# Optimization experiments

Hardware: AMD Instinct MI355X
Metric: run time of the kernel (lower is better)

The kernel has to match this reference:

```python
import jax, jax.numpy as jnp
import numpy as np

H = 512          # hidden_size
HALF = 256       # hidden_size // 2 (RGCN feature dim)
NHEAD = 8
NLAYER = 12
NBLOCK = 2
NENT = 50000
NREL = 12
NBASES = 8
NEDGE = 500000
TXTD = 768       # raw text/image feature dim
BATCH, ELEN, SLEN = 32, 50, 128


def setup_inputs() -> dict:
    key = jax.random.key(0)
    ks = jax.random.split(key, 40)
    def p(i, shape, scale=0.02):
        return jax.random.normal(ks[i], shape, jnp.float32) * scale
    inp = {
        'entity_ids': jax.random.randint(ks[0], (BATCH, ELEN), 0, NENT),
        'token_embeds': jax.random.normal(ks[1], (BATCH, SLEN, H), jnp.float32),
        'edge_index': jax.random.randint(ks[2], (2, NEDGE), 0, NENT),
        'edge_type': jax.random.randint(ks[3], (NEDGE,), 0, NREL),
        'node_embeds': p(4, (NENT, HALF)),
        'rgcn_basis': p(5, (NBASES, HALF, HALF)),
        'rgcn_comp': p(6, (NREL, NBASES), 0.3),
        'rgcn_root': p(7, (HALF, HALF)),
        'rgcn_bias': p(8, (HALF,)),
        'kg_proj_w': p(9, (HALF, H)), 'kg_proj_b': p(10, (H,)),
        'text_proj_w': p(11, (TXTD, H)), 'text_proj_b': p(12, (H,)),
        'image_proj_w': p(13, (TXTD, H)), 'image_proj_b': p(14, (H,)),
        'cq_w': p(15, (H, H)), 'cq_b': p(16, (H,)),
        'kgk_w': p(17, (H, H)), 'kgk_b': p(18, (H,)),
        'imk_w': p(19, (H, H)), 'imk_b': p(20, (H,)),
        'txk_w': p(21, (H, H)), 'txk_b': p(22, (H,)),
        'pp1_w1': p(23, (H, HALF)), 'pp1_b1': p(24, (HALF,)),
        'pp1_w2': p(25, (HALF, H)), 'pp1_b2': p(26, (H,)),
        'pp2_w': p(27, (H, NLAYER * NBLOCK * H)), 'pp2_b': p(28, (NLAYER * NBLOCK * H,)),
        'text_embeds_init': p(29, (NENT, TXTD), 1.0),
        'image_embeds_init': p(30, (NENT, TXTD), 1.0),
    }
    return inp


def _rgcn(x, edge_index, edge_type, basis, comp, root, bias):
    # PyG RGCNConv with basis decomposition, aggr='mean', root weight + bias.
    # mean_{e: rel=r, dst=i}(x[src_e] @ W_r) == (mean_{e}(x[src_e])) @ W_r, so we
    # aggregate raw features per (dst, relation) segment then apply W_r once per node.
    N = x.shape[0]
    src, dst = edge_index[0], edge_index[1]
    seg = dst * NREL + edge_type                      # combined (node, relation) key
    msgs = x[src]                                     # [E, HALF] gather
    agg = jax.ops.segment_sum(msgs, seg, num_segments=N * NREL)
    cnt = jax.ops.segment_sum(jnp.ones((src.shape[0],), x.dtype), seg, num_segments=N * NREL)
    mean = (agg / jnp.maximum(cnt, 1.0)[:, None]).reshape(N, NREL, HALF)
    w_rel = jnp.einsum('rb,bio->rio', comp, basis)    # [R, HALF, HALF]
    out = jnp.einsum('nri,rio->no', mean, w_rel) + x @ root + bias
    return out


def reference(entity_ids, token_embeds, edge_index, edge_type, node_embeds,
              rgcn_basis, rgcn_comp, rgcn_root, rgcn_bias,
              kg_proj_w, kg_proj_b, text_proj_w, text_proj_b,
              image_proj_w, image_proj_b, cq_w, cq_b,
              kgk_w, kgk_b, imk_w, imk_b, txk_w, txk_b,
              pp1_w1, pp1_b1, pp1_w2, pp1_b2, pp2_w, pp2_b,
              text_embeds_init, image_embeds_init):
    kg_all = _rgcn(node_embeds, edge_index, edge_type, rgcn_basis, rgcn_comp, rgcn_root, rgcn_bias)
    kg_all = kg_all @ kg_proj_w + kg_proj_b           # [N, H]
    kg_feat = kg_all[entity_ids]                      # [B, L, H]
    text_feat = text_embeds_init[entity_ids] @ text_proj_w + text_proj_b
    image_feat = image_embeds_init[entity_ids] @ image_proj_w + image_proj_b
    # context-guided fusion
    q = (jnp.mean(token_embeds, axis=1) @ cq_w + cq_b)[:, None, :]   # [B, 1, H]
    kg_s = jnp.sum(q * (kg_feat @ kgk_w + kgk_b), -1, keepdims=True)
    img_s = jnp.sum(q * (image_feat @ imk_w + imk_b), -1, keepdims=True)
    txt_s = jnp.sum(q * (text_feat @ txk_w + txk_b), -1, keepdims=True)
    w = jax.nn.softmax(jnp.concatenate([kg_s, img_s, txt_s], axis=-1), axis=-1)
    fused = w[..., 0:1] * kg_feat + w[..., 1:2] * image_feat + w[..., 2:3] * text_feat
    # prompt expansion
    h = jax.nn.relu(fused @ pp1_w1 + pp1_b1) @ pp1_w2 + pp1_b2 + fused
    p = h @ pp2_w + pp2_b                             # [B, L, NLAYER*NBLOCK*H]
    B, L = entity_ids.shape
    p = p.reshape(B, L, NLAYER, NBLOCK, NHEAD, H // NHEAD)
    p = jnp.transpose(p, (2, 3, 0, 4, 1, 5))          # [layer, block, B, head, L, head_dim]
    loss_cl = jnp.float32(0.0)                        # output_entity=False path
    return p, loss_cl
```

## Files before the change

kernel.cpp:

```cpp
#include <hip/hip_runtime.h>

#define HDIM 512
#define HALF 256
#define NRELS 12
#define NBASES 8
#define NLAYERS 12
#define NBLOCKS 2
#define NHEADS 8
#define NENTS 50000
#define TXTD 768
#define BATCH 32
#define ELEN 50
#define SLEN 128
#define NPOS (BATCH * ELEN)
#define NSEG (NPOS * NRELS)
#define BCAP 64

typedef unsigned short u16;
typedef __attribute__((ext_vector_type(8))) __bf16 bf16x8;
typedef __attribute__((ext_vector_type(4))) float f32x4;

__device__ __forceinline__ u16 f2bf(float f) {
    unsigned int u = __float_as_uint(f);
    unsigned int r = (u + 0x7FFFu + ((u >> 16) & 1u)) >> 16;
    return (u16)r;
}
__device__ __forceinline__ float bf2f(u16 v) {
    return __uint_as_float(((unsigned int)v) << 16);
}

#define ASYNC_COPY16(g, l)                                                              \
    __builtin_amdgcn_global_load_lds((const __attribute__((address_space(1))) void*)(g), \
                                     (__attribute__((address_space(3))) unsigned int*)(l), 16, 0, 0)

__global__ void init_kernel(int* __restrict__ map, int* __restrict__ segcnt,
                            int* __restrict__ nuniq, float* __restrict__ zb,
                            const float* __restrict__ kgb, const float* __restrict__ imb,
                            const float* __restrict__ txb, u16* __restrict__ SW,
                            const float* __restrict__ rgcn_bias,
                            const float* __restrict__ kg_proj_w,
                            const float* __restrict__ kg_proj_b,
                            float* __restrict__ biasC, float* __restrict__ out_last) {
    int blk = blockIdx.x;
    int t = threadIdx.x;
    if (blk >= 128) {
        int n = (blk - 128) * 256 + t;
        float acc = kg_proj_b[n];
        for (int c = 0; c < HALF; ++c) acc += rgcn_bias[c] * kg_proj_w[(size_t)c * HDIM + n];
        biasC[n] = acc;
        return;
    }
    int tid = blk * 256 + t;
    const int nt = 128 * 256;
    int4 m4 = {-1, -1, -1, -1};
    for (int i = tid; i < NENTS / 4; i += nt) ((int4*)map)[i] = m4;
    int4 z4 = {0, 0, 0, 0};
    for (int i = tid; i < NSEG / 4; i += nt) ((int4*)segcnt)[i] = z4;
    for (int i = tid; i < 2304; i += nt) zb[i] = 0.f;
    if (tid < HDIM) {
        SW[(size_t)1536 * HDIM + tid] = f2bf(kgb[tid]);
        SW[(size_t)1537 * HDIM + tid] = f2bf(imb[tid]);
        SW[(size_t)1538 * HDIM + tid] = f2bf(txb[tid]);
    }
    if (tid == 0) { *nuniq = 0; *out_last = 0.f; }
}

__global__ void dedup_kernel(const int* __restrict__ eid, int* __restrict__ map,
                             int* __restrict__ uniq, int* __restrict__ nuniq) {
    int i = blockIdx.x * blockDim.x + threadIdx.x;
    if (i >= NPOS) return;
    int n = eid[i];
    int old = atomicCAS(&map[n], -1, -2);
    if (old == -1) {
        int idx = atomicAdd(nuniq, 1);
        uniq[idx] = n;
        __threadfence();
        map[n] = idx;
    }
}

struct PrepArgs {
    const float* src[12];
    u16* dst[12];
};

__global__ __launch_bounds__(256) void midprep_kernel(
    const float* __restrict__ tok, u16* __restrict__ TMEAN,
    const int* __restrict__ uniq, const int* __restrict__ nuniq,
    const float* __restrict__ txi, const float* __restrict__ imi,
    u16* __restrict__ TXIN, u16* __restrict__ IMIN,
    const int* __restrict__ ei, const int* __restrict__ et, const int* __restrict__ map,
    int* __restrict__ segcnt, int* __restrict__ bucket, int E, PrepArgs a) {
    int blk = blockIdx.x;
    int t = threadIdx.x;
    if (blk < 64) {
        int b = blk >> 1;
        int col = (blk & 1) * 256 + t;
        float s = 0.f;
        for (int si = 0; si < SLEN; ++si) s += tok[((size_t)b * SLEN + si) * HDIM + col];
        TMEAN[(size_t)b * HDIM + col] = f2bf(s * (1.0f / SLEN));
    } else if (blk < 352) {
        if (t >= TXTD / 4) return;
        int nu = *nuniq;
        for (int u = blk - 64; u < NPOS; u += 288) {
            if (u >= nu) {
                ushort4 z = {0, 0, 0, 0};
                ((ushort4*)(TXIN + (size_t)u * TXTD))[t] = z;
                ((ushort4*)(IMIN + (size_t)u * TXTD))[t] = z;
                continue;
            }
            int n = uniq[u];
            float4 v = ((const float4*)(txi + (size_t)n * TXTD))[t];
            ushort4 o;
            o.x = f2bf(v.x); o.y = f2bf(v.y); o.z = f2bf(v.z); o.w = f2bf(v.w);
            ((ushort4*)(TXIN + (size_t)u * TXTD))[t] = o;
            v = ((const float4*)(imi + (size_t)n * TXTD))[t];
            o.x = f2bf(v.x); o.y = f2bf(v.y); o.z = f2bf(v.z); o.w = f2bf(v.w);
            ((ushort4*)(IMIN + (size_t)u * TXTD))[t] = o;
        }
    } else if (blk < 1024) {
        const int* __restrict__ dstA = ei + E;
        int tid0 = (blk - 352) * 256 + t;
        const int stride = 672 * 256;
        for (int e = tid0; e < E; e += stride) {
            int c = map[dstA[e]];
            if (c >= 0) {
                int seg = c * NRELS + et[e];
                int p = atomicAdd(&segcnt[seg], 1);
                if (p < BCAP) bucket[seg * BCAP + p] = ei[e];
            }
        }
    } else {
        constexpr int NN[7]  = {512, 512, 512, 256, 512, 12288, 512};
        constexpr int LDT[7] = {256, 768, 768, 512, 256, 512, 512};
        constexpr int BASE[13] = {0, 128, 512, 896, 1024, 1152, 7296,
                                  7552, 8064, 8128, 8384, 8640, 8896};
        __shared__ u16 tb[32][33];
        int bid = blk - 1024;
        int op = 0;
        #pragma unroll
        for (int i = 1; i < 12; ++i)
            if (bid >= BASE[i]) op = i;
        int idx = bid - BASE[op];
        if (op < 7) {
            int Nv = 0, ldt = 0;
            #pragma unroll
            for (int i = 0; i < 7; ++i)
                if (op == i) { Nv = NN[i]; ldt = LDT[i]; }
            int ncols = Nv / 32;
            int n0 = (idx % ncols) * 32, k0 = (idx / ncols) * 32;
            const float* W = a.src[op];
            u16* WT = a.dst[op];
            int tx = t & 31, ty = t >> 5;
            #pragma unroll
            for (int i = ty; i < 32; i += 8)
                tb[i][tx] = f2bf(W[(size_t)(k0 + i) * Nv + n0 + tx]);
            __syncthreads();
            #pragma unroll
            for (int i = ty; i < 32; i += 8)
                WT[(size_t)(n0 + i) * ldt + k0 + tx] = tb[tx][i];
        } else {
            int e = idx * 1024 + t * 4;
            float4 v = *(const float4*)(a.src[op] + e);
            ushort4 o;
            o.x = f2bf(v.x); o.y = f2bf(v.y); o.z = f2bf(v.z); o.w = f2bf(v.w);
            *(ushort4*)(a.dst[op] + e) = o;
        }
    }
}

template <int BM, int BN, int WM, int WN, bool SCATTER>
__device__ __forceinline__ void gemm_body(const u16* __restrict__ A, const u16* __restrict__ BT,
                                          const float* __restrict__ bias,
                                          void* __restrict__ Cout, int M, int N, int K,
                                          int bx, int by, bool outbf) {
    constexpr int MF = WM / 16, NF = WN / 16;
    constexpr int NWC = BN / WN;
    __shared__ u16 ldsA[BM][64];
    __shared__ u16 ldsB[BN][64];
    const int tid = threadIdx.x;
    const int lane = tid & 63;
    const int wv = tid >> 6;
    const int m0 = by * BM;
    const int n0 = bx * BN;
    const int wr = wv / NWC, wc = wv % NWC;
    const int srow = lane >> 3;
    const int sslot = lane & 7;

    f32x4 acc[MF][NF];
    #pragma unroll
    for (int i = 0; i < MF; ++i)
        #pragma unroll
        for (int j = 0; j < NF; ++j)
            #pragma unroll
            for (int r = 0; r < 4; ++r) acc[i][j][r] = 0.f;

    for (int k0 = 0; k0 < K; k0 += 64) {
        #pragma unroll
        for (int i = 0; i < BM / 32; ++i) {
            int R = wv * (BM / 4) + i * 8 + srow;
            int gm = m0 + R;
            gm = gm < M ? gm : M - 1;
            int s = sslot ^ (R & 7);
            ASYNC_COPY16(A + (size_t)gm * K + k0 + s * 8, &ldsA[wv * (BM / 4) + i * 8][0]);
        }
        #pragma unroll
        for (int i = 0; i < BN / 32; ++i) {
            int R = wv * (BN / 4) + i * 8 + srow;
            int s = sslot ^ (R & 7);
            ASYNC_COPY16(BT + (size_t)(n0 + R) * K + k0 + s * 8, &ldsB[wv * (BN / 4) + i * 8][0]);
        }
        __syncthreads();
        #pragma unroll
        for (int ks = 0; ks < 2; ++ks) {
            bf16x8 af[MF], bf[NF];
            int kg = ks * 4 + (lane >> 4);
            int rl = lane & 15;
            #pragma unroll
            for (int i = 0; i < MF; ++i) {
                int row = wr * WM + i * 16 + rl;
                af[i] = *(const bf16x8*)&ldsA[row][(kg ^ (row & 7)) * 8];
            }
            #pragma unroll
            for (int j = 0; j < NF; ++j) {
                int row = wc * WN + j * 16 + rl;
                bf[j] = *(const bf16x8*)&ldsB[row][(kg ^ (row & 7)) * 8];
            }
            #pragma unroll
            for (int i = 0; i < MF; ++i)
                #pragma unroll
                for (int j = 0; j < NF; ++j)
                    acc[i][j] = __builtin_amdgcn_mfma_f32_16x16x32_bf16(af[i], bf[j], acc[i][j], 0, 0, 0);
        }
        __syncthreads();
    }

    const int rl = lane & 15, rg = lane >> 4;
    #pragma unroll
    for (int i = 0; i < MF; ++i) {
        #pragma unroll
        for (int j = 0; j < NF; ++j) {
            int col = n0 + wc * WN + j * 16 + rl;
            float bv = bias[col];
            #pragma unroll
            for (int r = 0; r < 4; ++r) {
                int row = m0 + wr * WM + i * 16 + rg * 4 + r;
                if (row >= M) continue;
                float x = acc[i][j][r] + bv;
                if (SCATTER) {
                    int layer = col >> 10, blk = (col >> 9) & 1, head = (col >> 6) & 7, hd = col & 63;
                    int bb = row / ELEN, ll = row - bb * ELEN;
                    size_t oi = (((((size_t)layer * NBLOCKS + blk) * BATCH + bb) * NHEADS + head) * ELEN + ll) * 64 + hd;
                    ((float*)Cout)[oi] = x;
                } else if (outbf) {
                    ((u16*)Cout)[(size_t)row * N + col] = f2bf(x);
                } else {
                    ((float*)Cout)[(size_t)row * N + col] = x;
                }
            }
        }
    }
}

struct BuildArgs {
    const int *segcnt, *bucket, *uniq, *nuniq;
    const float *comp, *x;
    u16* MBX;
    const u16 *TMEAN, *CQT;
    const float* cq_b;
    u16* QB;
    const u16 *KGT, *W1f;
    const float* ZB;
    u16* WC;
    const u16 *TXIN, *TXT, *IMIN, *IMT;
    const float *txb, *imb;
    u16 *TXU, *IMU;
};
__global__ __launch_bounds__(256) void build_kernel(BuildArgs a) {
    int blk = blockIdx.x;
    if (blk >= NPOS) {
        const u16 *A, *BT;
        const float* bias;
        u16* C;
        int M, N, K, bx, by;
        if (blk >= NPOS + 8 + 288 + 200) {
            int i = blk - (NPOS + 8 + 288 + 200);
            A = a.IMIN; BT = a.IMT; bias = a.imb; C = a.IMU;
            M = NPOS; N = HDIM; K = TXTD; bx = i % 8; by = i / 8;
        } else if (blk >= NPOS + 8 + 288) {
            int i = blk - (NPOS + 8 + 288);
            A = a.TXIN; BT = a.TXT; bias = a.txb; C = a.TXU;
            M = NPOS; N = HDIM; K = TXTD; bx = i % 8; by = i / 8;
        } else if (blk >= NPOS + 8) {
            int i = blk - (NPOS + 8);
            A = a.KGT; BT = a.W1f; bias = a.ZB; C = a.WC;
            M = HDIM; N = 2304; K = HALF; bx = i % 36; by = i / 36;
        } else {
            A = a.TMEAN; BT = a.CQT; bias = a.cq_b; C = a.QB;
            M = BATCH; N = HDIM; K = HDIM; bx = blk - NPOS; by = 0;
        }
        gemm_body<64, 64, 32, 32, false>(A, BT, bias, C, M, N, K, bx, by, true);
        return;
    }
    int u = blk;
    int i = threadIdx.x;
    __shared__ float sc[NRELS * NBASES];
    if (i < NRELS * NBASES) sc[i] = a.comp[i];
    __syncthreads();
    u16* row = a.MBX + (size_t)u * 2304;
    int nu = *a.nuniq;
    if (u >= nu) {
        for (int b = 0; b < NBASES + 1; ++b) row[b * HALF + i] = 0;
        return;
    }
    float mr[NRELS];
    #pragma unroll
    for (int r = 0; r < NRELS; ++r) {
        int seg = u * NRELS + r;
        int c = a.segcnt[seg];
        int n = min(c, BCAP);
        float acc = 0.f;
        for (int e = 0; e < n; ++e) {
            int s = a.bucket[seg * BCAP + e];
            acc += a.x[(size_t)s * HALF + i];
        }
        mr[r] = acc * (1.f / fmaxf((float)c, 1.f));
    }
    #pragma unroll
    for (int b = 0; b < NBASES; ++b) {
        float v = 0.f;
        #pragma unroll
        for (int r = 0; r < NRELS; ++r) v += sc[r * NBASES + b] * mr[r];
        row[b * HALF + i] = f2bf(v);
    }
    row[NBASES * HALF + i] = f2bf(a.x[(size_t)a.uniq[u] * HALF + i]);
}

struct ProjArgs {
    const u16 *MBX, *WC, *QB, *SW;
    const float *biasC, *ZB;
    u16* KGU;
    float* QP;
};
__global__ __launch_bounds__(256) void proj_kernel(ProjArgs a) {
    int b = blockIdx.x;
    if (b < 200) {
        gemm_body<64, 64, 32, 32, false>(a.MBX, a.WC, a.biasC, a.KGU,
                                         NPOS, HDIM, 2304, b % 8, b / 8, true);
    } else {
        gemm_body<64, 64, 32, 32, false>(a.QB, a.SW, a.ZB, a.QP,
                                         BATCH, 1600, HDIM, b - 200, 0, false);
    }
}

__global__ __launch_bounds__(256) void tail_kernel(
    const int* __restrict__ eid, const int* __restrict__ map,
    const u16* __restrict__ KGU, const u16* __restrict__ IMU, const u16* __restrict__ TXU,
    const float* __restrict__ qp,
    const u16* __restrict__ W1T, const float* __restrict__ pp1_b1,
    const u16* __restrict__ W2T, const float* __restrict__ pp1_b2,
    u16* __restrict__ Hh) {
    __shared__ u16 FUS[16][520];
    __shared__ u16 P1s[16][264];
    const int bm0 = blockIdx.x * 16;
    const int lane = threadIdx.x & 63;
    const int wv = threadIdx.x >> 6;

    for (int rr = wv; rr < 16; rr += 4) {
        int bl = bm0 + rr;
        int b = bl / ELEN;
        int u = map[eid[bl]];
        const u16* kg = KGU + (size_t)u * HDIM;
        const u16* im = IMU + (size_t)u * HDIM;
        const u16* tx = TXU + (size_t)u * HDIM;
        const float* qrow = qp + (size_t)b * 1600;
        float pkg = 0.f, pim = 0.f, ptx = 0.f;
        for (int e = lane; e < HDIM; e += 64) {
            pkg += bf2f(kg[e]) * qrow[e];
            pim += bf2f(im[e]) * qrow[512 + e];
            ptx += bf2f(tx[e]) * qrow[1024 + e];
        }
        #pragma unroll
        for (int off = 32; off; off >>= 1) {
            pkg += __shfl_down(pkg, off);
            pim += __shfl_down(pim, off);
            ptx += __shfl_down(ptx, off);
        }
        float w0, w1, w2;
        if (lane == 0) {
            float av = pkg + qrow[1536];
            float c1 = pim + qrow[1537];
            float c2 = ptx + qrow[1538];
            float mx = fmaxf(av, fmaxf(c1, c2));
            float ea = __expf(av - mx), eb = __expf(c1 - mx), ec = __expf(c2 - mx);
            float inv = 1.f / (ea + eb + ec);
            w0 = ea * inv; w1 = eb * inv; w2 = ec * inv;
        }
        w0 = __shfl(w0, 0); w1 = __shfl(w1, 0); w2 = __shfl(w2, 0);
        for (int e = lane; e < HDIM; e += 64) {
            float v = w0 * bf2f(kg[e]) + w1 * bf2f(im[e]) + w2 * bf2f(tx[e]);
            FUS[rr][e] = f2bf(v);
        }
    }
    __syncthreads();

    {
        const int rl = lane & 15;
        const int kgrp = lane >> 4;
        f32x4 acc[4];
        #pragma unroll
        for (int j = 0; j < 4; ++j)
            #pragma unroll
            for (int r = 0; r < 4; ++r) acc[j][r] = 0.f;
        for (int kk = 0; kk < 512; kk += 32) {
            int k8 = kk + kgrp * 8;
            bf16x8 af = *(const bf16x8*)&FUS[rl][k8];
            bf16x8 bf[4];
            #pragma unroll
            for (int j = 0; j < 4; ++j) {
                int n = wv * 64 + j * 16 + rl;
                bf[j] = *(const bf16x8*)&W1T[(size_t)n * 512 + k8];
            }
            #pragma unroll
            for (int j = 0; j < 4; ++j)
                acc[j] = __builtin_amdgcn_mfma_f32_16x16x32_bf16(af, bf[j], acc[j], 0, 0, 0);
        }
        const int rg = lane >> 4;
        #pragma unroll
        for (int j = 0; j < 4; ++j) {
            int col = wv * 64 + j * 16 + rl;
            float bv = pp1_b1[col];
            #pragma unroll
            for (int r = 0; r < 4; ++r) {
                int row = rg * 4 + r;
                P1s[row][col] = f2bf(fmaxf(acc[j][r] + bv, 0.f));
            }
        }
    }
    __syncthreads();

    {
        const int rl = lane & 15;
        const int kgrp = lane >> 4;
        f32x4 acc[8];
        #pragma unroll
        for (int j = 0; j < 8; ++j)
            #pragma unroll
            for (int r = 0; r < 4; ++r) acc[j][r] = 0.f;
        for (int kk = 0; kk < 256; kk += 32) {
            int k8 = kk + kgrp * 8;
            bf16x8 af = *(const bf16x8*)&P1s[rl][k8];
            bf16x8 bf[8];
            #pragma unroll
            for (int j = 0; j < 8; ++j) {
                int n = wv * 128 + j * 16 + rl;
                bf[j] = *(const bf16x8*)&W2T[(size_t)n * 256 + k8];
            }
            #pragma unroll
            for (int j = 0; j < 8; ++j)
                acc[j] = __builtin_amdgcn_mfma_f32_16x16x32_bf16(af, bf[j], acc[j], 0, 0, 0);
        }
        const int rg = lane >> 4;
        #pragma unroll
        for (int j = 0; j < 8; ++j) {
            int col = wv * 128 + j * 16 + rl;
            float bv = pp1_b2[col];
            #pragma unroll
            for (int r = 0; r < 4; ++r) {
                int row = rg * 4 + r;
                float v = acc[j][r] + bv + bf2f(FUS[row][col]);
                Hh[(size_t)(bm0 + row) * HDIM + col] = f2bf(v);
            }
        }
    }
}

__global__ __launch_bounds__(256)
void pp2_kernel(const u16* __restrict__ A, const u16* __restrict__ BT,
                const float* __restrict__ bias, void* __restrict__ Cout,
                int M, int N, int K) {
    int id = blockIdx.x;
    int xcd = id & 7;
    int local = id >> 3;
    int bx = xcd * 12 + local % 12;
    int by = local / 12;
    gemm_body<128, 128, 64, 64, true>(A, BT, bias, Cout, M, N, K, bx, by, false);
}

extern "C" void kernel_launch(void* const* d_in, const int* in_sizes, int n_in,
                              void* d_out, int out_size, void* d_ws, size_t ws_size,
                              hipStream_t stream) {
    const int* entity_ids = (const int*)d_in[0];
    const float* token_embeds = (const float*)d_in[1];
    const int* edge_index = (const int*)d_in[2];
    const int* edge_type = (const int*)d_in[3];
    const float* node_embeds = (const float*)d_in[4];
    const float* rgcn_basis = (const float*)d_in[5];
    const float* rgcn_comp = (const float*)d_in[6];
    const float* rgcn_root = (const float*)d_in[7];
    const float* rgcn_bias = (const float*)d_in[8];
    const float* kg_proj_w = (const float*)d_in[9];
    const float* kg_proj_b = (const float*)d_in[10];
    const float* text_proj_w = (const float*)d_in[11];
    const float* text_proj_b = (const float*)d_in[12];
    const float* image_proj_w = (const float*)d_in[13];
    const float* image_proj_b = (const float*)d_in[14];
    const float* cq_w = (const float*)d_in[15];
    const float* cq_b = (const float*)d_in[16];
    const float* kgk_w = (const float*)d_in[17];
    const float* imk_w = (const float*)d_in[19];
    const float* txk_w = (const float*)d_in[21];
    const float* pp1_w1 = (const float*)d_in[23];
    const float* pp1_b1 = (const float*)d_in[24];
    const float* pp1_w2 = (const float*)d_in[25];
    const float* pp1_b2 = (const float*)d_in[26];
    const float* pp2_w = (const float*)d_in[27];
    const float* pp2_b = (const float*)d_in[28];
    const float* text_init = (const float*)d_in[29];
    const float* image_init = (const float*)d_in[30];

    const int E = in_sizes[3];

    size_t off = 0;
    auto alloc = [&](size_t bytes) { size_t o = off; off += (bytes + 255) & ~(size_t)255; return o; };
    char* ws = (char*)d_ws;
    size_t map_o  = alloc((size_t)NENTS * 4);
    size_t nun_o  = alloc(4);
    size_t unq_o  = alloc((size_t)NPOS * 4);
    size_t scnt_o = alloc((size_t)NSEG * 4);
    size_t bkt_o  = alloc((size_t)NSEG * BCAP * 4);
    size_t mbx_o  = alloc((size_t)NPOS * 2304 * 2);
    size_t w1f_o  = alloc((size_t)2304 * HALF * 2);
    size_t wc_o   = alloc((size_t)HDIM * 2304 * 2);
    size_t bc_o   = alloc((size_t)HDIM * 4);
    size_t kgt_o  = alloc((size_t)HDIM * HALF * 2);
    size_t kgu_o  = alloc((size_t)NPOS * HDIM * 2);
    size_t txin_o = alloc((size_t)NPOS * TXTD * 2);
    size_t imin_o = alloc((size_t)NPOS * TXTD * 2);
    size_t txt_o  = alloc((size_t)HDIM * TXTD * 2);
    size_t imt_o  = alloc((size_t)HDIM * TXTD * 2);
    size_t txu_o  = alloc((size_t)NPOS * HDIM * 2);
    size_t imu_o  = alloc((size_t)NPOS * HDIM * 2);
    size_t tm_o   = alloc((size_t)BATCH * HDIM * 2);
    size_t qb_o   = alloc((size_t)BATCH * HDIM * 2);
    size_t cqt_o  = alloc((size_t)HDIM * HDIM * 2);
    size_t sw_o   = alloc((size_t)1600 * HDIM * 2);
    size_t qp_o   = alloc((size_t)BATCH * 1600 * 4);
    size_t zb_o   = alloc((size_t)2304 * 4);
    size_t w1t_o  = alloc((size_t)HALF * HDIM * 2);
    size_t w2t_o  = alloc((size_t)HDIM * HALF * 2);
    size_t h_o    = alloc((size_t)NPOS * HDIM * 2);
    size_t pp2t_o = alloc((size_t)12288 * HDIM * 2);
    if (off > ws_size) return;

    int* map = (int*)(ws + map_o);
    int* nuniq = (int*)(ws + nun_o);
    int* uniq = (int*)(ws + unq_o);
    int* segcnt = (int*)(ws + scnt_o);
    int* bucket = (int*)(ws + bkt_o);
    u16* MBX = (u16*)(ws + mbx_o);
    u16* W1f = (u16*)(ws + w1f_o);
    u16* WC  = (u16*)(ws + wc_o);
    float* biasC = (float*)(ws + bc_o);
    u16* KGT = (u16*)(ws + kgt_o);
    u16* KGU = (u16*)(ws + kgu_o);
    u16* TXIN = (u16*)(ws + txin_o);
    u16* IMIN = (u16*)(ws + imin_o);
    u16* TXT = (u16*)(ws + txt_o);
    u16* IMT = (u16*)(ws + imt_o);
    u16* TXU = (u16*)(ws + txu_o);
    u16* IMU = (u16*)(ws + imu_o);
    u16* TMEAN = (u16*)(ws + tm_o);
    u16* QB  = (u16*)(ws + qb_o);
    u16* CQT = (u16*)(ws + cqt_o);
    u16* SW  = (u16*)(ws + sw_o);
    float* QP  = (float*)(ws + qp_o);
    float* ZB  = (float*)(ws + zb_o);
    u16* W1T = (u16*)(ws + w1t_o);
    u16* W2T = (u16*)(ws + w2t_o);
    u16* Hh  = (u16*)(ws + h_o);
    u16* PP2T = (u16*)(ws + pp2t_o);
    float* OUT = (float*)d_out;

    init_kernel<<<130, 256, 0, stream>>>(map, segcnt, nuniq, ZB,
                                         (const float*)d_in[18], (const float*)d_in[20],
                                         (const float*)d_in[22], SW,
                                         rgcn_bias, kg_proj_w, kg_proj_b, biasC,
                                         OUT + (out_size - 1));
    dedup_kernel<<<(NPOS + 255) / 256, 256, 0, stream>>>(entity_ids, map, uniq, nuniq);
    PrepArgs pa;
    pa.src[0] = kg_proj_w;    pa.dst[0] = KGT;
    pa.src[1] = text_proj_w;  pa.dst[1] = TXT;
    pa.src[2] = image_proj_w; pa.dst[2] = IMT;
    pa.src[3] = pp1_w1;       pa.dst[3] = W1T;
    pa.src[4] = pp1_w2;       pa.dst[4] = W2T;
    pa.src[5] = pp2_w;        pa.dst[5] = PP2T;
    pa.src[6] = cq_w;         pa.dst[6] = CQT;
    pa.src[7] = rgcn_basis;   pa.dst[7] = W1f;
    pa.src[8] = rgcn_root;    pa.dst[8] = W1f + (size_t)2048 * HALF;
    pa.src[9] = kgk_w;        pa.dst[9] = SW;
    pa.src[10] = imk_w;       pa.dst[10] = SW + (size_t)HDIM * HDIM;
    pa.src[11] = txk_w;       pa.dst[11] = SW + (size_t)2 * HDIM * HDIM;
    midprep_kernel<<<9920, 256, 0, stream>>>(token_embeds, TMEAN,
                                             uniq, nuniq, text_init, image_init, TXIN, IMIN,
                                             edge_index, edge_type, map, segcnt, bucket, E, pa);
    BuildArgs ba;
    ba.segcnt = segcnt; ba.bucket = bucket; ba.uniq = uniq; ba.nuniq = nuniq;
    ba.comp = rgcn_comp; ba.x = node_embeds; ba.MBX = MBX;
    ba.TMEAN = TMEAN; ba.CQT = CQT; ba.cq_b = cq_b; ba.QB = QB;
    ba.KGT = KGT; ba.W1f = W1f; ba.ZB = ZB; ba.WC = WC;
    ba.TXIN = TXIN; ba.TXT = TXT; ba.IMIN = IMIN; ba.IMT = IMT;
    ba.txb = text_proj_b; ba.imb = image_proj_b; ba.TXU = TXU; ba.IMU = IMU;
    build_kernel<<<NPOS + 8 + 288 + 400, 256, 0, stream>>>(ba);
    ProjArgs pr;
    pr.MBX = MBX; pr.WC = WC; pr.biasC = biasC; pr.KGU = KGU;
    pr.QB = QB; pr.SW = SW; pr.ZB = ZB; pr.QP = QP;
    proj_kernel<<<225, 256, 0, stream>>>(pr);
    tail_kernel<<<NPOS / 16, 256, 0, stream>>>(entity_ids, map, KGU, IMU, TXU, QP,
                                               W1T, pp1_b1, W2T, pp1_b2, Hh);
    pp2_kernel<<<1248, 256, 0, stream>>>(Hh, PP2T, pp2_b, OUT, NPOS, 12288, HDIM);
}
```

Before: 155.3 us.

## Replace dense entity map with shared-memory hash dedup and widen small GEMM blocks

Entity deduplication now happens in one block using a shared-memory open-addressing hash table. This removes the 50000-entry map initialization and the separate dedup kernel, and it writes a position-to-unique index array for the tail kernel. The edge bucketing step probes the 4096-slot global hash table instead of indexing the dense map, which adds probe loops per edge. The small GEMMs in the build and projection kernels move to 512-thread blocks with 8 waves over a 64x64 tile, each wave computing 32x16. The RGCN build path now exits its upper 256 threads early.

```diff
diff --git a/kernel.cpp b/kernel.cpp
--- a/kernel.cpp
+++ b/kernel.cpp
@@ -15,6 +15,7 @@
 #define NPOS (BATCH * ELEN)
 #define NSEG (NPOS * NRELS)
 #define BCAP 64
+#define HTSZ 4096
 
 typedef unsigned short u16;
 typedef __attribute__((ext_vector_type(8))) __bf16 bf16x8;
@@ -28,32 +29,70 @@
 __device__ __forceinline__ float bf2f(u16 v) {
     return __uint_as_float(((unsigned int)v) << 16);
 }
+__device__ __forceinline__ unsigned hash_ent(int n) {
+    return ((unsigned)n * 2654435761u) >> 20;
+}
 
 #define ASYNC_COPY16(g, l)                                                              \
     __builtin_amdgcn_global_load_lds((const __attribute__((address_space(1))) void*)(g), \
                                      (__attribute__((address_space(3))) unsigned int*)(l), 16, 0, 0)
 
-__global__ void init_kernel(int* __restrict__ map, int* __restrict__ segcnt,
-                            int* __restrict__ nuniq, float* __restrict__ zb,
-                            const float* __restrict__ kgb, const float* __restrict__ imb,
-                            const float* __restrict__ txb, u16* __restrict__ SW,
-                            const float* __restrict__ rgcn_bias,
-                            const float* __restrict__ kg_proj_w,
-                            const float* __restrict__ kg_proj_b,
-                            float* __restrict__ biasC, float* __restrict__ out_last) {
+__global__ __launch_bounds__(256) void init_kernel(
+    const int* __restrict__ eid, int* __restrict__ uniq, int* __restrict__ nuniq,
+    int* __restrict__ pos2u, int2* __restrict__ HT,
+    int* __restrict__ segcnt, float* __restrict__ zb,
+    const float* __restrict__ kgb, const float* __restrict__ imb,
+    const float* __restrict__ txb, u16* __restrict__ SW,
+    const float* __restrict__ rgcn_bias, const float* __restrict__ kg_proj_w,
+    const float* __restrict__ kg_proj_b, float* __restrict__ biasC,
+    float* __restrict__ out_last) {
     int blk = blockIdx.x;
     int t = threadIdx.x;
-    if (blk >= 128) {
-        int n = (blk - 128) * 256 + t;
+    if (blk == 0) {
+        __shared__ int hkey[HTSZ];
+        __shared__ int hval[HTSZ];
+        __shared__ int lcnt;
+        for (int i = t; i < HTSZ; i += 256) hkey[i] = -1;
+        if (t == 0) lcnt = 0;
+        __syncthreads();
+        for (int i = t; i < NPOS; i += 256) {
+            int n = eid[i];
+            unsigned h = hash_ent(n);
+            while (true) {
+                int old = atomicCAS(&hkey[h], -1, n);
+                if (old == -1) {
+                    int v = atomicAdd(&lcnt, 1);
+                    hval[h] = v;
+                    uniq[v] = n;
+                    break;
+                }
+                if (old == n) break;
+                h = (h + 1) & (HTSZ - 1);
+            }
+        }
+        __syncthreads();
+        for (int i = t; i < NPOS; i += 256) {
+            int n = eid[i];
+            unsigned h = hash_ent(n);
+            while (hkey[h] != n) h = (h + 1) & (HTSZ - 1);
+            pos2u[i] = hval[h];
+        }
+        for (int i = t; i < HTSZ; i += 256) {
+            int2 kv; kv.x = hkey[i]; kv.y = (hkey[i] == -1) ? -1 : hval[i];
+            HT[i] = kv;
+        }
+        if (t == 0) { *nuniq = lcnt; *out_last = 0.f; }
+        return;
+    }
+    if (blk <= 2) {
+        int n = (blk - 1) * 256 + t;
         float acc = kg_proj_b[n];
         for (int c = 0; c < HALF; ++c) acc += rgcn_bias[c] * kg_proj_w[(size_t)c * HDIM + n];
         biasC[n] = acc;
         return;
     }
-    int tid = blk * 256 + t;
-    const int nt = 128 * 256;
-    int4 m4 = {-1, -1, -1, -1};
-    for (int i = tid; i < NENTS / 4; i += nt) ((int4*)map)[i] = m4;
+    int tid = (blk - 3) * 256 + t;
+    const int nt = 31 * 256;
     int4 z4 = {0, 0, 0, 0};
     for (int i = tid; i < NSEG / 4; i += nt) ((int4*)segcnt)[i] = z4;
     for (int i = tid; i < 2304; i += nt) zb[i] = 0.f;
@@ -62,21 +101,6 @@
         SW[(size_t)1537 * HDIM + tid] = f2bf(imb[tid]);
         SW[(size_t)1538 * HDIM + tid] = f2bf(txb[tid]);
     }
-    if (tid == 0) { *nuniq = 0; *out_last = 0.f; }
-}
-
-__global__ void dedup_kernel(const int* __restrict__ eid, int* __restrict__ map,
-                             int* __restrict__ uniq, int* __restrict__ nuniq) {
-    int i = blockIdx.x * blockDim.x + threadIdx.x;
-    if (i >= NPOS) return;
-    int n = eid[i];
-    int old = atomicCAS(&map[n], -1, -2);
-    if (old == -1) {
-        int idx = atomicAdd(nuniq, 1);
-        uniq[idx] = n;
-        __threadfence();
-        map[n] = idx;
-    }
 }
 
 struct PrepArgs {
@@ -89,7 +113,8 @@
     const int* __restrict__ uniq, const int* __restrict__ nuniq,
     const float* __restrict__ txi, const float* __restrict__ imi,
     u16* __restrict__ TXIN, u16* __restrict__ IMIN,
-    const int* __restrict__ ei, const int* __restrict__ et, const int* __restrict__ map,
+    const int* __restrict__ ei, const int* __restrict__ et,
+    const int2* __restrict__ HT,
     int* __restrict__ segcnt, int* __restrict__ bucket, int E, PrepArgs a) {
     int blk = blockIdx.x;
     int t = threadIdx.x;
@@ -123,7 +148,15 @@
         int tid0 = (blk - 352) * 256 + t;
         const int stride = 672 * 256;
         for (int e = tid0; e < E; e += stride) {
-            int c = map[dstA[e]];
+            int d = dstA[e];
+            unsigned h = hash_ent(d);
+            int c = -1;
+            while (true) {
+                int2 kv = HT[h];
+                if (kv.x == d) { c = kv.y; break; }
+                if (kv.x == -1) break;
+                h = (h + 1) & (HTSZ - 1);
+            }
             if (c >= 0) {
                 int seg = c * NRELS + et[e];
                 int p = atomicAdd(&segcnt[seg], 1);
@@ -169,11 +202,80 @@
     }
 }
 
-template <int BM, int BN, int WM, int WN, bool SCATTER>
-__device__ __forceinline__ void gemm_body(const u16* __restrict__ A, const u16* __restrict__ BT,
-                                          const float* __restrict__ bias,
-                                          void* __restrict__ Cout, int M, int N, int K,
-                                          int bx, int by, bool outbf) {
+__device__ __forceinline__ void gemm_body512(const u16* __restrict__ A, const u16* __restrict__ BT,
+                                             const float* __restrict__ bias,
+                                             void* __restrict__ Cout, int M, int N, int K,
+                                             int bx, int by, bool outbf) {
+    __shared__ u16 ldsA[64][64];
+    __shared__ u16 ldsB[64][64];
+    const int tid = threadIdx.x;
+    const int lane = tid & 63;
+    const int wv = tid >> 6;
+    const int m0 = by * 64;
+    const int n0 = bx * 64;
+    const int wr = wv >> 2;
+    const int wc = wv & 3;
+    const int srow = lane >> 3;
+    const int sslot = lane & 7;
+
+    f32x4 acc[2];
+    #pragma unroll
+    for (int i = 0; i < 2; ++i)
+        #pragma unroll
+        for (int r = 0; r < 4; ++r) acc[i][r] = 0.f;
+
+    for (int k0 = 0; k0 < K; k0 += 64) {
+        {
+            int R = wv * 8 + srow;
+            int gm = m0 + R;
+            gm = gm < M ? gm : M - 1;
+            int s = sslot ^ (R & 7);
+            ASYNC_COPY16(A + (size_t)gm * K + k0 + s * 8, &ldsA[wv * 8][0]);
+            ASYNC_COPY16(BT + (size_t)(n0 + R) * K + k0 + s * 8, &ldsB[wv * 8][0]);
+        }
+        __syncthreads();
+        #pragma unroll
+        for (int ks = 0; ks < 2; ++ks) {
+            int kg = ks * 4 + (lane >> 4);
+            int rl = lane & 15;
+            bf16x8 af[2], bfr;
+            #pragma unroll
+            for (int i = 0; i < 2; ++i) {
+                int row = wr * 32 + i * 16 + rl;
+                af[i] = *(const bf16x8*)&ldsA[row][(kg ^ (row & 7)) * 8];
+            }
+            {
+                int row = wc * 16 + rl;
+                bfr = *(const bf16x8*)&ldsB[row][(kg ^ (row & 7)) * 8];
+            }
+            #pragma unroll
+            for (int i = 0; i < 2; ++i)
+                acc[i] = __builtin_amdgcn_mfma_f32_16x16x32_bf16(af[i], bfr, acc[i], 0, 0, 0);
+        }
+        __syncthreads();
+    }
+
+    const int rl = lane & 15, rg = lane >> 4;
+    int col = n0 + wc * 16 + rl;
+    float bv = bias[col];
+    #pragma unroll
+    for (int i = 0; i < 2; ++i) {
+        #pragma unroll
+        for (int r = 0; r < 4; ++r) {
+            int row = m0 + wr * 32 + i * 16 + rg * 4 + r;
+            if (row >= M) continue;
+            float x = acc[i][r] + bv;
+            if (outbf) ((u16*)Cout)[(size_t)row * N + col] = f2bf(x);
+            else       ((float*)Cout)[(size_t)row * N + col] = x;
+        }
+    }
+}
+
+__device__ __forceinline__ void gemm_body_pp2(const u16* __restrict__ A, const u16* __restrict__ BT,
+                                              const float* __restrict__ bias,
+                                              float* __restrict__ Cout, int M, int N, int K,
+                                              int bx, int by) {
+    constexpr int BM = 128, BN = 128, WM = 64, WN = 64;
     constexpr int MF = WM / 16, NF = WN / 16;
     constexpr int NWC = BN / WN;
     __shared__ u16 ldsA[BM][64];
@@ -247,16 +349,10 @@
                 int row = m0 + wr * WM + i * 16 + rg * 4 + r;
                 if (row >= M) continue;
                 float x = acc[i][j][r] + bv;
-                if (SCATTER) {
-                    int layer = col >> 10, blk = (col >> 9) & 1, head = (col >> 6) & 7, hd = col & 63;
-                    int bb = row / ELEN, ll = row - bb * ELEN;
-                    size_t oi = (((((size_t)layer * NBLOCKS + blk) * BATCH + bb) * NHEADS + head) * ELEN + ll) * 64 + hd;
-                    ((float*)Cout)[oi] = x;
-                } else if (outbf) {
-                    ((u16*)Cout)[(size_t)row * N + col] = f2bf(x);
-                } else {
-                    ((float*)Cout)[(size_t)row * N + col] = x;
-                }
+                int layer = col >> 10, blk = (col >> 9) & 1, head = (col >> 6) & 7, hd = col & 63;
+                int bb = row / ELEN, ll = row - bb * ELEN;
+                size_t oi = (((((size_t)layer * NBLOCKS + blk) * BATCH + bb) * NHEADS + head) * ELEN + ll) * 64 + hd;
+                Cout[oi] = x;
             }
         }
     }
@@ -276,7 +372,7 @@
     const float *txb, *imb;
     u16 *TXU, *IMU;
 };
-__global__ __launch_bounds__(256) void build_kernel(BuildArgs a) {
+__global__ __launch_bounds__(512) void build_kernel(BuildArgs a) {
     int blk = blockIdx.x;
     if (blk >= NPOS) {
         const u16 *A, *BT;
@@ -299,7 +395,7 @@
             A = a.TMEAN; BT = a.CQT; bias = a.cq_b; C = a.QB;
             M = BATCH; N = HDIM; K = HDIM; bx = blk - NPOS; by = 0;
         }
-        gemm_body<64, 64, 32, 32, false>(A, BT, bias, C, M, N, K, bx, by, true);
+        gemm_body512(A, BT, bias, C, M, N, K, bx, by, true);
         return;
     }
     int u = blk;
@@ -307,6 +403,7 @@
     __shared__ float sc[NRELS * NBASES];
     if (i < NRELS * NBASES) sc[i] = a.comp[i];
     __syncthreads();
+    if (i >= 256) return;
     u16* row = a.MBX + (size_t)u * 2304;
     int nu = *a.nuniq;
     if (u >= nu) {
@@ -342,19 +439,25 @@
     u16* KGU;
     float* QP;
 };
-__global__ __launch_bounds__(256) void proj_kernel(ProjArgs a) {
+__global__ __launch_bounds__(512) void proj_kernel(ProjArgs a) {
     int b = blockIdx.x;
+    const u16 *A, *BT;
+    const float* bias;
+    void* C;
+    int M, N, K, bx, by;
+    bool obf;
     if (b < 200) {
-        gemm_body<64, 64, 32, 32, false>(a.MBX, a.WC, a.biasC, a.KGU,
-                                         NPOS, HDIM, 2304, b % 8, b / 8, true);
+        A = a.MBX; BT = a.WC; bias = a.biasC; C = a.KGU;
+        M = NPOS; N = HDIM; K = 2304; bx = b % 8; by = b / 8; obf = true;
     } else {
-        gemm_body<64, 64, 32, 32, false>(a.QB, a.SW, a.ZB, a.QP,
-                                         BATCH, 1600, HDIM, b - 200, 0, false);
-    }
+        A = a.QB; BT = a.SW; bias = a.ZB; C = a.QP;
+        M = BATCH; N = 1600; K = HDIM; bx = b - 200; by = 0; obf = false;
+    }
+    gemm_body512(A, BT, bias, C, M, N, K, bx, by, obf);
 }
 
 __global__ __launch_bounds__(256) void tail_kernel(
-    const int* __restrict__ eid, const int* __restrict__ map,
+    const int* __restrict__ pos2u,
     const u16* __restrict__ KGU, const u16* __restrict__ IMU, const u16* __restrict__ TXU,
     const float* __restrict__ qp,
     const u16* __restrict__ W1T, const float* __restrict__ pp1_b1,
@@ -369,7 +472,7 @@
     for (int rr = wv; rr < 16; rr += 4) {
         int bl = bm0 + rr;
         int b = bl / ELEN;
-        int u = map[eid[bl]];
+        int u = pos2u[bl];
         const u16* kg = KGU + (size_t)u * HDIM;
         const u16* im = IMU + (size_t)u * HDIM;
         const u16* tx = TXU + (size_t)u * HDIM;
@@ -477,14 +580,14 @@
 
 __global__ __launch_bounds__(256)
 void pp2_kernel(const u16* __restrict__ A, const u16* __restrict__ BT,
-                const float* __restrict__ bias, void* __restrict__ Cout,
+                const float* __restrict__ bias, float* __restrict__ Cout,
                 int M, int N, int K) {
     int id = blockIdx.x;
     int xcd = id & 7;
     int local = id >> 3;
     int bx = xcd * 12 + local % 12;
     int by = local / 12;
-    gemm_body<128, 128, 64, 64, true>(A, BT, bias, Cout, M, N, K, bx, by, false);
+    gemm_body_pp2(A, BT, bias, Cout, M, N, K, bx, by);
 }
 
 extern "C" void kernel_launch(void* const* d_in, const int* in_sizes, int n_in,
@@ -524,9 +627,10 @@
     size_t off = 0;
     auto alloc = [&](size_t bytes) { size_t o = off; off += (bytes + 255) & ~(size_t)255; return o; };
     char* ws = (char*)d_ws;
-    size_t map_o  = alloc((size_t)NENTS * 4);
     size_t nun_o  = alloc(4);
     size_t unq_o  = alloc((size_t)NPOS * 4);
+    size_t p2u_o  = alloc((size_t)NPOS * 4);
+    size_t ht_o   = alloc((size_t)HTSZ * 8);
     size_t scnt_o = alloc((size_t)NSEG * 4);
     size_t bkt_o  = alloc((size_t)NSEG * BCAP * 4);
     size_t mbx_o  = alloc((size_t)NPOS * 2304 * 2);
@@ -553,9 +657,10 @@
     size_t pp2t_o = alloc((size_t)12288 * HDIM * 2);
     if (off > ws_size) return;
 
-    int* map = (int*)(ws + map_o);
     int* nuniq = (int*)(ws + nun_o);
     int* uniq = (int*)(ws + unq_o);
+    int* pos2u = (int*)(ws + p2u_o);
+    int2* HT = (int2*)(ws + ht_o);
     int* segcnt = (int*)(ws + scnt_o);
     int* bucket = (int*)(ws + bkt_o);
     u16* MBX = (u16*)(ws + mbx_o);
@@ -582,12 +687,12 @@
     u16* PP2T = (u16*)(ws + pp2t_o);
     float* OUT = (float*)d_out;
 
-    init_kernel<<<130, 256, 0, stream>>>(map, segcnt, nuniq, ZB,
-                                         (const float*)d_in[18], (const float*)d_in[20],
-                                         (const float*)d_in[22], SW,
-                                         rgcn_bias, kg_proj_w, kg_proj_b, biasC,
-                                         OUT + (out_size - 1));
-    dedup_kernel<<<(NPOS + 255) / 256, 256, 0, stream>>>(entity_ids, map, uniq, nuniq);
+    init_kernel<<<34, 256, 0, stream>>>(entity_ids, uniq, nuniq, pos2u, HT,
+                                        segcnt, ZB,
+                                        (const float*)d_in[18], (const float*)d_in[20],
+                                        (const float*)d_in[22], SW,
+                                        rgcn_bias, kg_proj_w, kg_proj_b, biasC,
+                                        OUT + (out_size - 1));
     PrepArgs pa;
     pa.src[0] = kg_proj_w;    pa.dst[0] = KGT;
     pa.src[1] = text_proj_w;  pa.dst[1] = TXT;
@@ -603,7 +708,7 @@
     pa.src[11] = txk_w;       pa.dst[11] = SW + (size_t)2 * HDIM * HDIM;
     midprep_kernel<<<9920, 256, 0, stream>>>(token_embeds, TMEAN,
                                              uniq, nuniq, text_init, image_init, TXIN, IMIN,
-                                             edge_index, edge_type, map, segcnt, bucket, E, pa);
+                                             edge_index, edge_type, HT, segcnt, bucket, E, pa);
     BuildArgs ba;
     ba.segcnt = segcnt; ba.bucket = bucket; ba.uniq = uniq; ba.nuniq = nuniq;
     ba.comp = rgcn_comp; ba.x = node_embeds; ba.MBX = MBX;
@@ -611,12 +716,12 @@
     ba.KGT = KGT; ba.W1f = W1f; ba.ZB = ZB; ba.WC = WC;
     ba.TXIN = TXIN; ba.TXT = TXT; ba.IMIN = IMIN; ba.IMT = IMT;
     ba.txb = text_proj_b; ba.imb = image_proj_b; ba.TXU = TXU; ba.IMU = IMU;
-    build_kernel<<<NPOS + 8 + 288 + 400, 256, 0, stream>>>(ba);
+    build_kernel<<<NPOS + 8 + 288 + 400, 512, 0, stream>>>(ba);
     ProjArgs pr;
     pr.MBX = MBX; pr.WC = WC; pr.biasC = biasC; pr.KGU = KGU;
     pr.QB = QB; pr.SW = SW; pr.ZB = ZB; pr.QP = QP;
-    proj_kernel<<<225, 256, 0, stream>>>(pr);
-    tail_kernel<<<NPOS / 16, 256, 0, stream>>>(entity_ids, map, KGU, IMU, TXU, QP,
+    proj_kernel<<<225, 512, 0, stream>>>(pr);
+    tail_kernel<<<NPOS / 16, 256, 0, stream>>>(pos2u, KGU, IMU, TXU, QP,
                                                W1T, pp1_b1, W2T, pp1_b2, Hh);
     pp2_kernel<<<1248, 256, 0, stream>>>(Hh, PP2T, pp2_b, OUT, NPOS, 12288, HDIM);
 }
```

Measured after the change: 158.3 us. About the same (+1.9%).
